# Optimization experiments

Measured on AMD Instinct MI355X. Metric: run time of the kernel, lower is better.

The kernel has to match this reference:

```python
import jax, jax.numpy as jnp
import numpy as np

DIM = 512
HEADS = 8
HEAD_DIM = DIM // HEADS

def setup_inputs() -> dict:
    key = jax.random.key(0)
    ks = jax.random.split(key, 5)
    s = 1.0 / np.sqrt(DIM)
    x = jax.random.normal(ks[0], (4, 2048, DIM), dtype=jnp.float32)
    w_qkv = jax.random.uniform(ks[1], (DIM, 3 * DIM), jnp.float32, -s, s)
    b_qkv = jax.random.uniform(ks[2], (3 * DIM,), jnp.float32, -s, s)
    w_out = jax.random.uniform(ks[3], (DIM, DIM), jnp.float32, -s, s)
    b_out = jax.random.uniform(ks[4], (DIM,), jnp.float32, -s, s)
    return {"x": x, "w_qkv": w_qkv, "b_qkv": b_qkv, "w_out": w_out, "b_out": b_out}

def reference(x, w_qkv, b_qkv, w_out, b_out):
    B, N, D = x.shape
    qkv = x @ w_qkv + b_qkv  # [B, N, 3D]
    qkv = qkv.reshape(B, N, 3, HEADS, HEAD_DIM).transpose(2, 0, 3, 1, 4)  # [3, B, H, N, hd]
    q, k, v = qkv[0], qkv[1], qkv[2]
    scale = 1.0 / np.sqrt(HEAD_DIM).astype(np.float32)
    attn = jnp.einsum('bhqd,bhkd->bhqk', q, k) * scale
    attn = jax.nn.softmax(attn, axis=-1)
    out = jnp.einsum('bhqk,bhkd->bhqd', attn, v)  # [B, H, N, hd]
    out = out.transpose(0, 2, 1, 3).reshape(B, N, D)
    return out @ w_out + b_out
```

## Files before the change

kernel.cpp:

```cpp
#include <hip/hip_runtime.h>

#define NB 4
#define NH 8
#define HD 64
#define DIMV 512
#define NSEQ 2048
#define QKVLD 1536
#define NTOK (NB*NSEQ)
#define KVB 64
#define QSCALE 0.18033688011112042f

typedef __attribute__((ext_vector_type(8))) short s8v;
typedef __attribute__((ext_vector_type(4))) float f4v;

typedef __attribute__((address_space(1))) void gvoid;
typedef __attribute__((address_space(3))) void lvoid;

__device__ __forceinline__ void load_lds16(const void* g, void* l){
  __builtin_amdgcn_global_load_lds((gvoid*)(void*)g, (lvoid*)l, 16, 0, 0);
}

__device__ __forceinline__ ushort f2bf(float f){
  unsigned u = __float_as_uint(f);
  u += 0x7fffu + ((u >> 16) & 1u);
  return (ushort)(u >> 16);
}

__device__ __forceinline__ unsigned pk2bf(float a, float b){
  return (unsigned)f2bf(a) | ((unsigned)f2bf(b) << 16);
}

__device__ __forceinline__ unsigned cvt_pk_bf16(float lo, float hi){
  unsigned r;
  asm("v_cvt_pk_bf16_f32 %0, %1, %2" : "=v"(r) : "v"(lo), "v"(hi));
  return r;
}
__device__ __forceinline__ float fexp2(float x){
  float r;
  asm("v_exp_f32 %0, %1" : "=v"(r) : "v"(x));
  return r;
}
__device__ __forceinline__ void plane32(unsigned &a, unsigned &b){
  asm("v_permlane32_swap_b32 %0, %1" : "+v"(a), "+v"(b));
}
__device__ __forceinline__ void plane16(unsigned &a, unsigned &b){
  asm("v_permlane16_swap_b32 %0, %1" : "+v"(a), "+v"(b));
}

__global__ __launch_bounds__(256) void k_prep(const float* __restrict__ x,
                                              ushort* __restrict__ xb,
                                              const float* __restrict__ w_qkv,
                                              ushort* __restrict__ wqkvT,
                                              const float* __restrict__ w_out,
                                              ushort* __restrict__ woutT){
  const int blk = blockIdx.x;
  const int tid = threadIdx.x;
  if (blk < 4096){
    const int i = blk * 256 + tid;
    float4 v = ((const float4*)x)[i];
    ushort4 o;
    o.x = f2bf(v.x); o.y = f2bf(v.y); o.z = f2bf(v.z); o.w = f2bf(v.w);
    ((ushort4*)xb)[i] = o;
    return;
  }
  __shared__ float t[32][33];
  const float* in; ushort* out; int C, bx, by;
  if (blk < 4864){
    const int idx = blk - 4096;
    in = w_qkv; out = wqkvT; C = QKVLD;
    bx = (idx % 48) * 32; by = (idx / 48) * 32;
  } else {
    const int idx = blk - 4864;
    in = w_out; out = woutT; C = DIMV;
    bx = (idx & 15) * 32; by = (idx >> 4) * 32;
  }
  const int tx = tid & 31, ty = tid >> 5;
  #pragma unroll
  for (int j = 0; j < 32; j += 8)
    t[ty + j][tx] = in[(size_t)(by + ty + j)*C + bx + tx];
  __syncthreads();
  #pragma unroll
  for (int j = 0; j < 32; j += 8)
    out[(size_t)(bx + ty + j)*DIMV + by + tx] = f2bf(t[tx][ty + j]);
}

template<bool SWAP>
__device__ __forceinline__ void gemm1_kloop(const ushort* __restrict__ A,
                                            const ushort* __restrict__ Bt,
                                            ushort* As, ushort* Bs,
                                            int tm, int tn, int K,
                                            int w, int l, int lr, int lg,
                                            f4v acc[2][4]){
  const int r8 = l >> 3;
  const int lc = (l & 7) ^ r8;
  const int swz = (lr & 7) << 4;
  const int wm = w >> 1, wn = w & 1;
  for (int kk = 0; kk < K; kk += 64){
    __syncthreads();
    #pragma unroll
    for (int c = 0; c < 2; ++c){
      const int ci = w*2 + c;
      const int row = ci*8 + r8;
      load_lds16(A + (size_t)(tm + row)*K + kk + lc*8, (char*)As + ci*1024);
    }
    #pragma unroll
    for (int c = 0; c < 4; ++c){
      const int ci = w*4 + c;
      const int row = ci*8 + r8;
      load_lds16(Bt + (size_t)(tn + row)*K + kk + lc*8, (char*)Bs + ci*1024);
    }
    __syncthreads();
    s8v af[2][2], bf[4][2];
    #pragma unroll
    for (int i = 0; i < 2; ++i){
      const int ra = (wm*32 + i*16 + lr)*128;
      #pragma unroll
      for (int t = 0; t < 2; ++t)
        af[i][t] = *(const s8v*)((const char*)As + ra + ((t*64 + lg*16) ^ swz));
    }
    #pragma unroll
    for (int i = 0; i < 4; ++i){
      const int rb = (wn*64 + i*16 + lr)*128;
      #pragma unroll
      for (int t = 0; t < 2; ++t)
        bf[i][t] = *(const s8v*)((const char*)Bs + rb + ((t*64 + lg*16) ^ swz));
    }
    #pragma unroll
    for (int mi = 0; mi < 2; ++mi)
      #pragma unroll
      for (int ni = 0; ni < 4; ++ni){
        if (SWAP){
          acc[mi][ni] = __builtin_amdgcn_mfma_f32_16x16x32_bf16(bf[ni][0], af[mi][0], acc[mi][ni], 0, 0, 0);
          acc[mi][ni] = __builtin_amdgcn_mfma_f32_16x16x32_bf16(bf[ni][1], af[mi][1], acc[mi][ni], 0, 0, 0);
        } else {
          acc[mi][ni] = __builtin_amdgcn_mfma_f32_16x16x32_bf16(af[mi][0], bf[ni][0], acc[mi][ni], 0, 0, 0);
          acc[mi][ni] = __builtin_amdgcn_mfma_f32_16x16x32_bf16(af[mi][1], bf[ni][1], acc[mi][ni], 0, 0, 0);
        }
      }
  }
}

template<int NCT>
__global__ __launch_bounds__(256) void k_gemm(const ushort* __restrict__ A,
                                              const ushort* __restrict__ Bt,
                                              const float* __restrict__ bias,
                                              void* __restrict__ Cout,
                                              ushort* __restrict__ vtp,
                                              int N, int K){
  __shared__ ushort As[64*64];
  __shared__ ushort Bs[128*64];
  const int tid = threadIdx.x;
  const int w = tid >> 6, l = tid & 63;
  const int lr = l & 15, lg = l >> 4;
  const int wm = w >> 1, wn = w & 1;
  const int wg = blockIdx.x;
  const int xcd = wg & 7, idx = wg >> 3;
  const int tn = (idx % NCT) * 128;
  const int tm = (xcd * 16 + idx / NCT) * 64;
  f4v acc[2][4] = {};

  if (tn >= 2*DIMV){
    gemm1_kloop<false>(A, Bt, As, Bs, tm, tn, K, w, l, lr, lg, acc);
    const int b = tm >> 11;
    const int n0 = (tm & (NSEQ-1)) + wm*32;
    #pragma unroll
    for (int ni = 0; ni < 4; ++ni){
      const int c = tn + wn*64 + ni*16 + lr;
      const int hd_i = c - 2*DIMV;
      const float bv = bias[c];
      ushort* vrow = vtp + ((size_t)(b*DIMV + hd_i))*NSEQ;
      #pragma unroll
      for (int mi = 0; mi < 2; ++mi){
        const int n = n0 + mi*16 + lg*4;
        uint2 pk;
        pk.x = pk2bf(acc[mi][ni][0] + bv, acc[mi][ni][1] + bv);
        pk.y = pk2bf(acc[mi][ni][2] + bv, acc[mi][ni][3] + bv);
        *(uint2*)(vrow + n) = pk;
      }
    }
    return;
  }

  gemm1_kloop<true>(A, Bt, As, Bs, tm, tn, K, w, l, lr, lg, acc);

  ushort* C = (ushort*)Cout;
  const float sc = (tn < DIMV) ? QSCALE : 1.0f;
  #pragma unroll
  for (int ni = 0; ni < 4; ++ni){
    const int c0 = tn + wn*64 + ni*16 + lg*4;
    const float4 bv = *(const float4*)(bias + c0);
    #pragma unroll
    for (int mi = 0; mi < 2; ++mi){
      const int r = tm + wm*32 + mi*16 + lr;
      uint2 pk;
      pk.x = pk2bf((acc[mi][ni][0] + bv.x)*sc, (acc[mi][ni][1] + bv.y)*sc);
      pk.y = pk2bf((acc[mi][ni][2] + bv.z)*sc, (acc[mi][ni][3] + bv.w)*sc);
      *(uint2*)(C + (size_t)r*N + c0) = pk;
    }
  }
}

__global__ __launch_bounds__(256) void k_gemm2(const ushort* __restrict__ A,
                                               const ushort* __restrict__ Bt,
                                               const float* __restrict__ bias,
                                               float* __restrict__ Cout){
  __shared__ ushort As[128*64];
  __shared__ ushort Bs[64*64];
  const int tid = threadIdx.x;
  const int w = tid >> 6, l = tid & 63;
  const int lr = l & 15, lg = l >> 4;
  const int wm = w >> 1, wn = w & 1;
  const int wg = blockIdx.x;
  const int xcd = wg & 7, idx = wg >> 3;
  const int tn = (idx & 7) * 64;
  const int tm = (xcd * 8 + (idx >> 3)) * 128;
  const int K = DIMV;
  const int r8 = l >> 3;
  const int lc = (l & 7) ^ r8;
  const int swz = (lr & 7) << 4;
  f4v acc[4][2] = {};

  for (int kk = 0; kk < K; kk += 64){
    __syncthreads();
    #pragma unroll
    for (int c = 0; c < 4; ++c){
      const int ci = w*4 + c;
      const int row = ci*8 + r8;
      load_lds16(A + (size_t)(tm + row)*K + kk + lc*8, (char*)As + ci*1024);
    }
    #pragma unroll
    for (int c = 0; c < 2; ++c){
      const int ci = w*2 + c;
      const int row = ci*8 + r8;
      load_lds16(Bt + (size_t)(tn + row)*K + kk + lc*8, (char*)Bs + ci*1024);
    }
    __syncthreads();
    s8v af[4][2], bf[2][2];
    #pragma unroll
    for (int i = 0; i < 4; ++i){
      const int ra = (wm*64 + i*16 + lr)*128;
      #pragma unroll
      for (int t = 0; t < 2; ++t)
        af[i][t] = *(const s8v*)((const char*)As + ra + ((t*64 + lg*16) ^ swz));
    }
    #pragma unroll
    for (int i = 0; i < 2; ++i){
      const int rb = (wn*32 + i*16 + lr)*128;
      #pragma unroll
      for (int t = 0; t < 2; ++t)
        bf[i][t] = *(const s8v*)((const char*)Bs + rb + ((t*64 + lg*16) ^ swz));
    }
    #pragma unroll
    for (int mi = 0; mi < 4; ++mi)
      #pragma unroll
      for (int ni = 0; ni < 2; ++ni){
        acc[mi][ni] = __builtin_amdgcn_mfma_f32_16x16x32_bf16(bf[ni][0], af[mi][0], acc[mi][ni], 0, 0, 0);
        acc[mi][ni] = __builtin_amdgcn_mfma_f32_16x16x32_bf16(bf[ni][1], af[mi][1], acc[mi][ni], 0, 0, 0);
      }
  }

  #pragma unroll
  for (int ni = 0; ni < 2; ++ni){
    const int c0 = tn + wn*32 + ni*16 + lg*4;
    const float4 bv = *(const float4*)(bias + c0);
    #pragma unroll
    for (int mi = 0; mi < 4; ++mi){
      const int r = tm + wm*64 + mi*16 + lr;
      float4 st;
      st.x = acc[mi][ni][0] + bv.x;
      st.y = acc[mi][ni][1] + bv.y;
      st.z = acc[mi][ni][2] + bv.z;
      st.w = acc[mi][ni][3] + bv.w;
      *(float4*)(Cout + (size_t)r*DIMV + c0) = st;
    }
  }
}

__global__ __launch_bounds__(256, 2) void k_attn(const ushort* __restrict__ qkv,
                                                 const ushort* __restrict__ vt,
                                                 ushort* __restrict__ ao){
  __shared__ alignas(1024) char smem[2][16384];
  const int tid = threadIdx.x;
  const int w = tid >> 6, l = tid & 63;
  const int lr = l & 15, lg = l >> 4;
  const int wg = blockIdx.x;
  const int n = (wg & 7) * 64 + (wg >> 3);
  const int bh = n >> 4, xt = n & 15;
  const int b = bh >> 3, h = bh & 7;
  const int q0 = xt * 128 + w * 32;

  const ushort* qpA = qkv + (size_t)(b*NSEQ + q0 + lr)*QKVLD + h*HD + lg*8;
  const ushort* qpB = qpA + (size_t)16*QKVLD;
  const s8v qfA0 = *(const s8v*)(qpA);
  const s8v qfA1 = *(const s8v*)(qpA + 32);
  const s8v qfB0 = *(const s8v*)(qpB);
  const s8v qfB1 = *(const s8v*)(qpB + 32);

  const int r8 = l >> 3;
  const int lc = (l & 7) ^ r8;
  const int wbase = w * 16;
  const ushort* kg0 = qkv + (size_t)(b*NSEQ + wbase + r8)*QKVLD + DIMV + h*HD + lc*8;
  const ushort* kg1 = kg0 + (size_t)8*QKVLD;
  const ushort* vg0 = vt + (size_t)(bh*HD + wbase + r8)*NSEQ + lc*8;
  const ushort* vg1 = vg0 + (size_t)8*NSEQ;

  float lsumA = 0.0f, lsumB = 0.0f;
  f4v oA[4] = {}, oB[4] = {};

  load_lds16(kg0, &smem[0][ wbase   *128]);
  load_lds16(kg1, &smem[0][(wbase+8)*128]);
  load_lds16(vg0, &smem[0][ wbase   *128 + 8192]);
  load_lds16(vg1, &smem[0][(wbase+8)*128 + 8192]);
  kg0 += (size_t)KVB*QKVLD; kg1 += (size_t)KVB*QKVLD; vg0 += KVB; vg1 += KVB;

  const int swz = (lr & 7) << 4;
  const int ro0 = lr*128 + ((     lg*16) ^ swz);
  const int ro1 = lr*128 + ((64 + lg*16) ^ swz);

  for (int kt = 0; kt < NSEQ/KVB; ++kt){
    const int cur = kt & 1;
    __syncthreads();

    if (kt + 1 < NSEQ/KVB){
      char* dst = &smem[cur^1][0];
      load_lds16(kg0, dst +  wbase   *128);
      load_lds16(kg1, dst + (wbase+8)*128);
      load_lds16(vg0, dst +  wbase   *128 + 8192);
      load_lds16(vg1, dst + (wbase+8)*128 + 8192);
      kg0 += (size_t)KVB*QKVLD; kg1 += (size_t)KVB*QKVLD; vg0 += KVB; vg1 += KVB;
    }

    const char* b0 = &smem[cur][0] + ro0;
    const char* b1 = &smem[cur][0] + ro1;

    f4v sA[4] = {}, sB[4] = {};
    __builtin_amdgcn_s_setprio(1);
    #pragma unroll
    for (int kb = 0; kb < 4; ++kb){
      const s8v kf0 = *(const s8v*)(b0 + kb*2048);
      const s8v kf1 = *(const s8v*)(b1 + kb*2048);
      sA[kb] = __builtin_amdgcn_mfma_f32_16x16x32_bf16(kf0, qfA0, sA[kb], 0,0,0);
      sA[kb] = __builtin_amdgcn_mfma_f32_16x16x32_bf16(kf1, qfA1, sA[kb], 0,0,0);
      sB[kb] = __builtin_amdgcn_mfma_f32_16x16x32_bf16(kf0, qfB0, sB[kb], 0,0,0);
      sB[kb] = __builtin_amdgcn_mfma_f32_16x16x32_bf16(kf1, qfB1, sB[kb], 0,0,0);
    }
    __builtin_amdgcn_s_setprio(0);

    union { uint4 u; s8v v; } pfA0, pfA1, pfB0, pfB1;
    {
      const float p0 = fexp2(sA[0][0]), p1 = fexp2(sA[0][1]);
      const float p2 = fexp2(sA[0][2]), p3 = fexp2(sA[0][3]);
      const float p4 = fexp2(sA[1][0]), p5 = fexp2(sA[1][1]);
      const float p6 = fexp2(sA[1][2]), p7 = fexp2(sA[1][3]);
      lsumA += ((p0 + p1) + (p2 + p3)) + ((p4 + p5) + (p6 + p7));
      unsigned a = cvt_pk_bf16(p0, p1), bq = cvt_pk_bf16(p4, p5);
      plane32(a, bq); plane16(a, bq);
      unsigned c = cvt_pk_bf16(p2, p3), d = cvt_pk_bf16(p6, p7);
      plane32(c, d);  plane16(c, d);
      pfA0.u.x = a; pfA0.u.y = c; pfA0.u.z = bq; pfA0.u.w = d;
    }
    {
      const float p0 = fexp2(sA[2][0]), p1 = fexp2(sA[2][1]);
      const float p2 = fexp2(sA[2][2]), p3 = fexp2(sA[2][3]);
      const float p4 = fexp2(sA[3][0]), p5 = fexp2(sA[3][1]);
      const float p6 = fexp2(sA[3][2]), p7 = fexp2(sA[3][3]);
      lsumA += ((p0 + p1) + (p2 + p3)) + ((p4 + p5) + (p6 + p7));
      unsigned a = cvt_pk_bf16(p0, p1), bq = cvt_pk_bf16(p4, p5);
      plane32(a, bq); plane16(a, bq);
      unsigned c = cvt_pk_bf16(p2, p3), d = cvt_pk_bf16(p6, p7);
      plane32(c, d);  plane16(c, d);
      pfA1.u.x = a; pfA1.u.y = c; pfA1.u.z = bq; pfA1.u.w = d;
    }
    {
      const float p0 = fexp2(sB[0][0]), p1 = fexp2(sB[0][1]);
      const float p2 = fexp2(sB[0][2]), p3 = fexp2(sB[0][3]);
      const float p4 = fexp2(sB[1][0]), p5 = fexp2(sB[1][1]);
      const float p6 = fexp2(sB[1][2]), p7 = fexp2(sB[1][3]);
      lsumB += ((p0 + p1) + (p2 + p3)) + ((p4 + p5) + (p6 + p7));
      unsigned a = cvt_pk_bf16(p0, p1), bq = cvt_pk_bf16(p4, p5);
      plane32(a, bq); plane16(a, bq);
      unsigned c = cvt_pk_bf16(p2, p3), d = cvt_pk_bf16(p6, p7);
      plane32(c, d);  plane16(c, d);
      pfB0.u.x = a; pfB0.u.y = c; pfB0.u.z = bq; pfB0.u.w = d;
    }
    {
      const float p0 = fexp2(sB[2][0]), p1 = fexp2(sB[2][1]);
      const float p2 = fexp2(sB[2][2]), p3 = fexp2(sB[2][3]);
      const float p4 = fexp2(sB[3][0]), p5 = fexp2(sB[3][1]);
      const float p6 = fexp2(sB[3][2]), p7 = fexp2(sB[3][3]);
      lsumB += ((p0 + p1) + (p2 + p3)) + ((p4 + p5) + (p6 + p7));
      unsigned a = cvt_pk_bf16(p0, p1), bq = cvt_pk_bf16(p4, p5);
      plane32(a, bq); plane16(a, bq);
      unsigned c = cvt_pk_bf16(p2, p3), d = cvt_pk_bf16(p6, p7);
      plane32(c, d);  plane16(c, d);
      pfB1.u.x = a; pfB1.u.y = c; pfB1.u.z = bq; pfB1.u.w = d;
    }

    __builtin_amdgcn_s_setprio(1);
    #pragma unroll
    for (int ni = 0; ni < 4; ++ni){
      const s8v vf0 = *(const s8v*)(b0 + 8192 + ni*2048);
      const s8v vf1 = *(const s8v*)(b1 + 8192 + ni*2048);
      oA[ni] = __builtin_amdgcn_mfma_f32_16x16x32_bf16(vf0, pfA0.v, oA[ni], 0,0,0);
      oA[ni] = __builtin_amdgcn_mfma_f32_16x16x32_bf16(vf1, pfA1.v, oA[ni], 0,0,0);
      oB[ni] = __builtin_amdgcn_mfma_f32_16x16x32_bf16(vf0, pfB0.v, oB[ni], 0,0,0);
      oB[ni] = __builtin_amdgcn_mfma_f32_16x16x32_bf16(vf1, pfB1.v, oB[ni], 0,0,0);
    }
    __builtin_amdgcn_s_setprio(0);
  }

  float ltA = lsumA;
  ltA += __shfl_xor(ltA, 16, 64);
  ltA += __shfl_xor(ltA, 32, 64);
  float ltB = lsumB;
  ltB += __shfl_xor(ltB, 16, 64);
  ltB += __shfl_xor(ltB, 32, 64);
  const float invA = 1.0f / ltA;
  const float invB = 1.0f / ltB;
  ushort* opA = ao + (size_t)(b*NSEQ + q0 + lr)*DIMV + h*HD;
  ushort* opB = opA + (size_t)16*DIMV;
  #pragma unroll
  for (int ni = 0; ni < 4; ++ni){
    uint2 pk;
    pk.x = cvt_pk_bf16(oA[ni][0]*invA, oA[ni][1]*invA);
    pk.y = cvt_pk_bf16(oA[ni][2]*invA, oA[ni][3]*invA);
    *(uint2*)(opA + ni*16 + lg*4) = pk;
    pk.x = cvt_pk_bf16(oB[ni][0]*invB, oB[ni][1]*invB);
    pk.y = cvt_pk_bf16(oB[ni][2]*invB, oB[ni][3]*invB);
    *(uint2*)(opB + ni*16 + lg*4) = pk;
  }
}


extern "C" void kernel_launch(void* const* d_in, const int* in_sizes, int n_in,
                              void* d_out, int out_size, void* d_ws, size_t ws_size,
                              hipStream_t stream) {
  (void)in_sizes; (void)n_in; (void)out_size; (void)ws_size;
  const float* x     = (const float*)d_in[0];
  const float* w_qkv = (const float*)d_in[1];
  const float* b_qkv = (const float*)d_in[2];
  const float* w_out = (const float*)d_in[3];
  const float* b_out = (const float*)d_in[4];
  float* out = (float*)d_out;

  char* ws = (char*)d_ws;
  ushort* xb    = (ushort*)(ws);
  ushort* wqkvT = (ushort*)(ws + 8388608);
  ushort* woutT = (ushort*)(ws + 8388608 + 1572864);
  ushort* qkv   = (ushort*)(ws + 10485760);
  ushort* vt    = (ushort*)(ws + 35651584);
  ushort* ao    = (ushort*)(ws + 44040192);

  k_prep<<<dim3(4096 + 768 + 256), 256, 0, stream>>>(x, xb, w_qkv, wqkvT, w_out, woutT);
  k_gemm<12><<<dim3(1536), 256, 0, stream>>>(xb, wqkvT, b_qkv, qkv, vt, QKVLD, DIMV);
  k_attn<<<dim3(512), 256, 0, stream>>>(qkv, vt, ao);
  k_gemm2<<<dim3(512), 256, 0, stream>>>(ao, woutT, b_out, out);
}
```

Before: 85.09 us.

## Process 64 query rows per wave in attention to increase K/V reuse

Each wave now computes 4 query blocks of 16 rows instead of 2, so each workgroup covers 256 queries and the grid halves to 256 workgroups. K and V fragments are loaded from LDS once per tile and reused across four query blocks, which cuts LDS traffic and K/V global loads per unit of work. In exchange, register pressure rises (launch bounds relaxed to one block) and the smaller grid lowers occupancy and latency hiding across CUs.

```diff
diff --git a/kernel.cpp b/kernel.cpp
--- a/kernel.cpp
+++ b/kernel.cpp
@@ -5,8 +5,8 @@
 #define HD 64
 #define DIMV 512
 #define NSEQ 2048
+#define NTOK (NB*NSEQ)
 #define QKVLD 1536
-#define NTOK (NB*NSEQ)
 #define KVB 64
 #define QSCALE 0.18033688011112042f
 
@@ -276,7 +276,7 @@
   }
 }
 
-__global__ __launch_bounds__(256, 2) void k_attn(const ushort* __restrict__ qkv,
+__global__ __launch_bounds__(256, 1) void k_attn(const ushort* __restrict__ qkv,
                                                  const ushort* __restrict__ vt,
                                                  ushort* __restrict__ ao){
   __shared__ alignas(1024) char smem[2][16384];
@@ -284,17 +284,18 @@
   const int w = tid >> 6, l = tid & 63;
   const int lr = l & 15, lg = l >> 4;
   const int wg = blockIdx.x;
-  const int n = (wg & 7) * 64 + (wg >> 3);
-  const int bh = n >> 4, xt = n & 15;
+  const int n = (wg & 7) * 32 + (wg >> 3);
+  const int bh = n >> 3, qt = n & 7;
   const int b = bh >> 3, h = bh & 7;
-  const int q0 = xt * 128 + w * 32;
-
-  const ushort* qpA = qkv + (size_t)(b*NSEQ + q0 + lr)*QKVLD + h*HD + lg*8;
-  const ushort* qpB = qpA + (size_t)16*QKVLD;
-  const s8v qfA0 = *(const s8v*)(qpA);
-  const s8v qfA1 = *(const s8v*)(qpA + 32);
-  const s8v qfB0 = *(const s8v*)(qpB);
-  const s8v qfB1 = *(const s8v*)(qpB + 32);
+  const int q0 = qt * 256 + w * 64;
+
+  s8v qf[4][2];
+  #pragma unroll
+  for (int qb = 0; qb < 4; ++qb){
+    const ushort* qp = qkv + (size_t)(b*NSEQ + q0 + qb*16 + lr)*QKVLD + h*HD + lg*8;
+    qf[qb][0] = *(const s8v*)(qp);
+    qf[qb][1] = *(const s8v*)(qp + 32);
+  }
 
   const int r8 = l >> 3;
   const int lc = (l & 7) ^ r8;
@@ -304,8 +305,8 @@
   const ushort* vg0 = vt + (size_t)(bh*HD + wbase + r8)*NSEQ + lc*8;
   const ushort* vg1 = vg0 + (size_t)8*NSEQ;
 
-  float lsumA = 0.0f, lsumB = 0.0f;
-  f4v oA[4] = {}, oB[4] = {};
+  float lsum[4] = {};
+  f4v o[4][4] = {};
 
   load_lds16(kg0, &smem[0][ wbase   *128]);
   load_lds16(kg1, &smem[0][(wbase+8)*128]);
@@ -333,101 +334,84 @@
     const char* b0 = &smem[cur][0] + ro0;
     const char* b1 = &smem[cur][0] + ro1;
 
-    f4v sA[4] = {}, sB[4] = {};
+    s8v kf[4][2];
+    #pragma unroll
+    for (int kb = 0; kb < 4; ++kb){
+      kf[kb][0] = *(const s8v*)(b0 + kb*2048);
+      kf[kb][1] = *(const s8v*)(b1 + kb*2048);
+    }
+    f4v s[4][4];
     __builtin_amdgcn_s_setprio(1);
     #pragma unroll
-    for (int kb = 0; kb < 4; ++kb){
-      const s8v kf0 = *(const s8v*)(b0 + kb*2048);
-      const s8v kf1 = *(const s8v*)(b1 + kb*2048);
-      sA[kb] = __builtin_amdgcn_mfma_f32_16x16x32_bf16(kf0, qfA0, sA[kb], 0,0,0);
-      sA[kb] = __builtin_amdgcn_mfma_f32_16x16x32_bf16(kf1, qfA1, sA[kb], 0,0,0);
-      sB[kb] = __builtin_amdgcn_mfma_f32_16x16x32_bf16(kf0, qfB0, sB[kb], 0,0,0);
-      sB[kb] = __builtin_amdgcn_mfma_f32_16x16x32_bf16(kf1, qfB1, sB[kb], 0,0,0);
-    }
+    for (int qb = 0; qb < 4; ++qb)
+      #pragma unroll
+      for (int kb = 0; kb < 4; ++kb){
+        f4v z = {0.f,0.f,0.f,0.f};
+        z = __builtin_amdgcn_mfma_f32_16x16x32_bf16(kf[kb][0], qf[qb][0], z, 0,0,0);
+        s[qb][kb] = __builtin_amdgcn_mfma_f32_16x16x32_bf16(kf[kb][1], qf[qb][1], z, 0,0,0);
+      }
     __builtin_amdgcn_s_setprio(0);
 
-    union { uint4 u; s8v v; } pfA0, pfA1, pfB0, pfB1;
-    {
-      const float p0 = fexp2(sA[0][0]), p1 = fexp2(sA[0][1]);
-      const float p2 = fexp2(sA[0][2]), p3 = fexp2(sA[0][3]);
-      const float p4 = fexp2(sA[1][0]), p5 = fexp2(sA[1][1]);
-      const float p6 = fexp2(sA[1][2]), p7 = fexp2(sA[1][3]);
-      lsumA += ((p0 + p1) + (p2 + p3)) + ((p4 + p5) + (p6 + p7));
-      unsigned a = cvt_pk_bf16(p0, p1), bq = cvt_pk_bf16(p4, p5);
-      plane32(a, bq); plane16(a, bq);
-      unsigned c = cvt_pk_bf16(p2, p3), d = cvt_pk_bf16(p6, p7);
-      plane32(c, d);  plane16(c, d);
-      pfA0.u.x = a; pfA0.u.y = c; pfA0.u.z = bq; pfA0.u.w = d;
-    }
-    {
-      const float p0 = fexp2(sA[2][0]), p1 = fexp2(sA[2][1]);
-      const float p2 = fexp2(sA[2][2]), p3 = fexp2(sA[2][3]);
-      const float p4 = fexp2(sA[3][0]), p5 = fexp2(sA[3][1]);
-      const float p6 = fexp2(sA[3][2]), p7 = fexp2(sA[3][3]);
-      lsumA += ((p0 + p1) + (p2 + p3)) + ((p4 + p5) + (p6 + p7));
-      unsigned a = cvt_pk_bf16(p0, p1), bq = cvt_pk_bf16(p4, p5);
-      plane32(a, bq); plane16(a, bq);
-      unsigned c = cvt_pk_bf16(p2, p3), d = cvt_pk_bf16(p6, p7);
-      plane32(c, d);  plane16(c, d);
-      pfA1.u.x = a; pfA1.u.y = c; pfA1.u.z = bq; pfA1.u.w = d;
-    }
-    {
-      const float p0 = fexp2(sB[0][0]), p1 = fexp2(sB[0][1]);
-      const float p2 = fexp2(sB[0][2]), p3 = fexp2(sB[0][3]);
-      const float p4 = fexp2(sB[1][0]), p5 = fexp2(sB[1][1]);
-      const float p6 = fexp2(sB[1][2]), p7 = fexp2(sB[1][3]);
-      lsumB += ((p0 + p1) + (p2 + p3)) + ((p4 + p5) + (p6 + p7));
-      unsigned a = cvt_pk_bf16(p0, p1), bq = cvt_pk_bf16(p4, p5);
-      plane32(a, bq); plane16(a, bq);
-      unsigned c = cvt_pk_bf16(p2, p3), d = cvt_pk_bf16(p6, p7);
-      plane32(c, d);  plane16(c, d);
-      pfB0.u.x = a; pfB0.u.y = c; pfB0.u.z = bq; pfB0.u.w = d;
-    }
-    {
-      const float p0 = fexp2(sB[2][0]), p1 = fexp2(sB[2][1]);
-      const float p2 = fexp2(sB[2][2]), p3 = fexp2(sB[2][3]);
-      const float p4 = fexp2(sB[3][0]), p5 = fexp2(sB[3][1]);
-      const float p6 = fexp2(sB[3][2]), p7 = fexp2(sB[3][3]);
-      lsumB += ((p0 + p1) + (p2 + p3)) + ((p4 + p5) + (p6 + p7));
-      unsigned a = cvt_pk_bf16(p0, p1), bq = cvt_pk_bf16(p4, p5);
-      plane32(a, bq); plane16(a, bq);
-      unsigned c = cvt_pk_bf16(p2, p3), d = cvt_pk_bf16(p6, p7);
-      plane32(c, d);  plane16(c, d);
-      pfB1.u.x = a; pfB1.u.y = c; pfB1.u.z = bq; pfB1.u.w = d;
-    }
-
+    union { uint4 u; s8v v; } pf[4][2];
+    #pragma unroll
+    for (int qb = 0; qb < 4; ++qb){
+      {
+        const float p0 = fexp2(s[qb][0][0]), p1 = fexp2(s[qb][0][1]);
+        const float p2 = fexp2(s[qb][0][2]), p3 = fexp2(s[qb][0][3]);
+        const float p4 = fexp2(s[qb][1][0]), p5 = fexp2(s[qb][1][1]);
+        const float p6 = fexp2(s[qb][1][2]), p7 = fexp2(s[qb][1][3]);
+        lsum[qb] += ((p0 + p1) + (p2 + p3)) + ((p4 + p5) + (p6 + p7));
+        unsigned a = cvt_pk_bf16(p0, p1), bq = cvt_pk_bf16(p4, p5);
+        plane32(a, bq); plane16(a, bq);
+        unsigned c = cvt_pk_bf16(p2, p3), d = cvt_pk_bf16(p6, p7);
+        plane32(c, d);  plane16(c, d);
+        pf[qb][0].u.x = a; pf[qb][0].u.y = c; pf[qb][0].u.z = bq; pf[qb][0].u.w = d;
+      }
+      {
+        const float p0 = fexp2(s[qb][2][0]), p1 = fexp2(s[qb][2][1]);
+        const float p2 = fexp2(s[qb][2][2]), p3 = fexp2(s[qb][2][3]);
+        const float p4 = fexp2(s[qb][3][0]), p5 = fexp2(s[qb][3][1]);
+        const float p6 = fexp2(s[qb][3][2]), p7 = fexp2(s[qb][3][3]);
+        lsum[qb] += ((p0 + p1) + (p2 + p3)) + ((p4 + p5) + (p6 + p7));
+        unsigned a = cvt_pk_bf16(p0, p1), bq = cvt_pk_bf16(p4, p5);
+        plane32(a, bq); plane16(a, bq);
+        unsigned c = cvt_pk_bf16(p2, p3), d = cvt_pk_bf16(p6, p7);
+        plane32(c, d);  plane16(c, d);
+        pf[qb][1].u.x = a; pf[qb][1].u.y = c; pf[qb][1].u.z = bq; pf[qb][1].u.w = d;
+      }
+    }
+
+    s8v vf[4][2];
+    #pragma unroll
+    for (int ni = 0; ni < 4; ++ni){
+      vf[ni][0] = *(const s8v*)(b0 + 8192 + ni*2048);
+      vf[ni][1] = *(const s8v*)(b1 + 8192 + ni*2048);
+    }
     __builtin_amdgcn_s_setprio(1);
     #pragma unroll
+    for (int ni = 0; ni < 4; ++ni)
+      #pragma unroll
+      for (int qb = 0; qb < 4; ++qb){
+        o[qb][ni] = __builtin_amdgcn_mfma_f32_16x16x32_bf16(vf[ni][0], pf[qb][0].v, o[qb][ni], 0,0,0);
+        o[qb][ni] = __builtin_amdgcn_mfma_f32_16x16x32_bf16(vf[ni][1], pf[qb][1].v, o[qb][ni], 0,0,0);
+      }
+    __builtin_amdgcn_s_setprio(0);
+  }
+
+  #pragma unroll
+  for (int qb = 0; qb < 4; ++qb){
+    float lt = lsum[qb];
+    lt += __shfl_xor(lt, 16, 64);
+    lt += __shfl_xor(lt, 32, 64);
+    const float inv = 1.0f / lt;
+    ushort* op = ao + (size_t)(b*NSEQ + q0 + qb*16 + lr)*DIMV + h*HD;
+    #pragma unroll
     for (int ni = 0; ni < 4; ++ni){
-      const s8v vf0 = *(const s8v*)(b0 + 8192 + ni*2048);
-      const s8v vf1 = *(const s8v*)(b1 + 8192 + ni*2048);
-      oA[ni] = __builtin_amdgcn_mfma_f32_16x16x32_bf16(vf0, pfA0.v, oA[ni], 0,0,0);
-      oA[ni] = __builtin_amdgcn_mfma_f32_16x16x32_bf16(vf1, pfA1.v, oA[ni], 0,0,0);
-      oB[ni] = __builtin_amdgcn_mfma_f32_16x16x32_bf16(vf0, pfB0.v, oB[ni], 0,0,0);
-      oB[ni] = __builtin_amdgcn_mfma_f32_16x16x32_bf16(vf1, pfB1.v, oB[ni], 0,0,0);
-    }
-    __builtin_amdgcn_s_setprio(0);
-  }
-
-  float ltA = lsumA;
-  ltA += __shfl_xor(ltA, 16, 64);
-  ltA += __shfl_xor(ltA, 32, 64);
-  float ltB = lsumB;
-  ltB += __shfl_xor(ltB, 16, 64);
-  ltB += __shfl_xor(ltB, 32, 64);
-  const float invA = 1.0f / ltA;
-  const float invB = 1.0f / ltB;
-  ushort* opA = ao + (size_t)(b*NSEQ + q0 + lr)*DIMV + h*HD;
-  ushort* opB = opA + (size_t)16*DIMV;
-  #pragma unroll
-  for (int ni = 0; ni < 4; ++ni){
-    uint2 pk;
-    pk.x = cvt_pk_bf16(oA[ni][0]*invA, oA[ni][1]*invA);
-    pk.y = cvt_pk_bf16(oA[ni][2]*invA, oA[ni][3]*invA);
-    *(uint2*)(opA + ni*16 + lg*4) = pk;
-    pk.x = cvt_pk_bf16(oB[ni][0]*invB, oB[ni][1]*invB);
-    pk.y = cvt_pk_bf16(oB[ni][2]*invB, oB[ni][3]*invB);
-    *(uint2*)(opB + ni*16 + lg*4) = pk;
+      uint2 pk;
+      pk.x = cvt_pk_bf16(o[qb][ni][0]*inv, o[qb][ni][1]*inv);
+      pk.y = cvt_pk_bf16(o[qb][ni][2]*inv, o[qb][ni][3]*inv);
+      *(uint2*)(op + ni*16 + lg*4) = pk;
+    }
   }
 }
 
@@ -453,6 +437,6 @@
 
   k_prep<<<dim3(4096 + 768 + 256), 256, 0, stream>>>(x, xb, w_qkv, wqkvT, w_out, woutT);
   k_gemm<12><<<dim3(1536), 256, 0, stream>>>(xb, wqkvT, b_qkv, qkv, vt, QKVLD, DIMV);
-  k_attn<<<dim3(512), 256, 0, stream>>>(qkv, vt, ao);
+  k_attn<<<dim3(256), 256, 0, stream>>>(qkv, vt, ao);
   k_gemm2<<<dim3(512), 256, 0, stream>>>(ao, woutT, b_out, out);
 }
```

After: 95.43 us. 1.12x slower.
